# Optimization experiments

Measured on AMD Instinct MI355X. Metric: run time of the kernel, lower is better.

## Reference

```python
import jax, jax.numpy as jnp
import numpy as np

EPS_PHI = 1e-18  # weight assigned to neighbors outside the support radius


def setup_inputs() -> dict:
    key = jax.random.key(0)
    k1, k2, k3, k4 = jax.random.split(key, 4)
    N, P, K = 2, 100000, 60
    points = jax.random.normal(k1, (N, P, 3), dtype=jnp.float32)
    v = jax.random.normal(k2, (N, P, K, 3), dtype=jnp.float32)
    vn = jax.random.normal(k3, (N, P, K, 3), dtype=jnp.float32)
    # squared support radii: positive, bounded away from zero
    sr = jax.random.uniform(k4, (N, P, K), dtype=jnp.float32) + 0.1
    return {"points": points, "v": v, "vn": vn, "sr": sr}


def reference(points, v, vn, sr):
    # points: (N,P,3); v,vn: (N,P,K,3); sr: (N,P,K)
    p_v = points[:, :, None, :] - v                      # (N,P,K,3)
    dists = jnp.sum(p_v * p_v, axis=-1)                  # (N,P,K) squared distances
    inside = dists < sr                                  # (N,P,K)
    w = 1.0 - dists / sr
    phi_v = jnp.where(inside, (w * w) * (w * w), EPS_PHI)  # quartic kernel weight
    v_to_p_dot_n = jnp.sum(vn * p_v, axis=-1)            # (N,P,K)
    sdf = jnp.sum(phi_v * v_to_p_dot_n, axis=-1) / jnp.sum(phi_v, axis=-1)  # (N,P)
    return jnp.sum(sdf * sdf, axis=-1)                   # (N,)
```

## Files before the change

kernel.cpp:

```cpp
#include <hip/hip_runtime.h>

#define SLOTS 256

__global__ __launch_bounds__(256) void sdf_main(
    const float* __restrict__ points,
    const float* __restrict__ v,
    const float* __restrict__ vn,
    const float* __restrict__ sr,
    float* __restrict__ ws,
    int NP, int K, int P)
{
    const int wave = blockIdx.x * 4 + (threadIdx.x >> 6);
    const int lane = threadIdx.x & 63;
    if (wave >= NP) return;

    const float px = points[wave * 3 + 0];
    const float py = points[wave * 3 + 1];
    const float pz = points[wave * 3 + 2];

    float num = 0.0f, den = 0.0f;
    if (lane < K) {
        const int base = (wave * K + lane) * 3;
        const float vx = v[base + 0];
        const float vy = v[base + 1];
        const float vz = v[base + 2];
        const float nx = vn[base + 0];
        const float ny = vn[base + 1];
        const float nz = vn[base + 2];
        const float s  = sr[wave * K + lane];

        const float dx = px - vx;
        const float dy = py - vy;
        const float dz = pz - vz;
        const float d2 = dx * dx + dy * dy + dz * dz;
        const float w  = 1.0f - d2 / s;
        const float w2 = w * w;
        const float phi = (d2 < s) ? (w2 * w2) : 1e-18f;
        const float dot = nx * dx + ny * dy + nz * dz;
        num = phi * dot;
        den = phi;
    }

    #pragma unroll
    for (int off = 32; off >= 1; off >>= 1) {
        num += __shfl_xor(num, off, 64);
        den += __shfl_xor(den, off, 64);
    }

    if (lane == 0) {
        const float sdf = num / den;
        const int n = wave / P;
        const int slot = wave & (SLOTS - 1);
        atomicAdd(&ws[slot * 2 + n], sdf * sdf);
    }
}

__global__ __launch_bounds__(512) void sdf_reduce(
    const float* __restrict__ ws, float* __restrict__ out, int N)
{
    __shared__ float sm[2 * SLOTS];
    const int tid  = threadIdx.x;
    const int n    = tid >> 8;
    const int slot = tid & (SLOTS - 1);
    sm[tid] = (n < N) ? ws[slot * 2 + n] : 0.0f;
    __syncthreads();
    #pragma unroll
    for (int s = SLOTS / 2; s >= 1; s >>= 1) {
        if (slot < s) sm[tid] += sm[tid + s];
        __syncthreads();
    }
    if (slot == 0 && n < N) out[n] = sm[tid];
}

extern "C" void kernel_launch(void* const* d_in, const int* in_sizes, int n_in,
                              void* d_out, int out_size, void* d_ws, size_t ws_size,
                              hipStream_t stream) {
    const float* points = (const float*)d_in[0];
    const float* v      = (const float*)d_in[1];
    const float* vn     = (const float*)d_in[2];
    const float* sr     = (const float*)d_in[3];
    float* out = (float*)d_out;
    float* ws  = (float*)d_ws;

    const int NP = in_sizes[0] / 3;
    const int K  = in_sizes[3] / NP;
    const int N  = out_size;
    const int P  = NP / N;

    hipMemsetAsync(ws, 0, SLOTS * 2 * sizeof(float), stream);

    const int waves_needed = NP;
    const int blocks = (waves_needed + 3) / 4;
    sdf_main<<<blocks, 256, 0, stream>>>(points, v, vn, sr, ws, NP, K, P);
    sdf_reduce<<<1, 2 * SLOTS, 0, stream>>>(ws, out, N);
}
```

Baseline: 382.5 us.

## Stage neighbor data via coalesced float4 loads into LDS and pad atomic slots

Each wave now loads its point's v, vn and sr rows as contiguous float4 vectors into shared memory, then reads the strided xyz components from LDS. This replaces the stride-3 scalar global loads. The atomic accumulation buffer grows to 512 slots with a 64-byte stride to reduce atomic contention and false sharing, and the reduce kernel loops over the slots. K is hardcoded to 60, and a block-wide barrier is added.

```diff
diff --git a/kernel.cpp b/kernel.cpp
--- a/kernel.cpp
+++ b/kernel.cpp
@@ -1,6 +1,6 @@
 #include <hip/hip_runtime.h>
 
-#define SLOTS 256
+#define RED_THREADS 512
 
 __global__ __launch_bounds__(256) void sdf_main(
     const float* __restrict__ points,
@@ -8,33 +8,55 @@
     const float* __restrict__ vn,
     const float* __restrict__ sr,
     float* __restrict__ ws,
-    int NP, int K, int P)
+    int NP, int P, int slots, int slotStride)
 {
-    const int wave = blockIdx.x * 4 + (threadIdx.x >> 6);
-    const int lane = threadIdx.x & 63;
-    if (wave >= NP) return;
+    constexpr int K = 60;
+    __shared__ float4 sv[4][45];
+    __shared__ float4 sn[4][45];
+    __shared__ float4 ss[4][15];
 
-    const float px = points[wave * 3 + 0];
-    const float py = points[wave * 3 + 1];
-    const float pz = points[wave * 3 + 2];
+    const int w     = threadIdx.x >> 6;
+    const int lane  = threadIdx.x & 63;
+    const int point = blockIdx.x * 4 + w;
+    const bool active = point < NP;
 
-    float num = 0.0f, den = 0.0f;
-    if (lane < K) {
-        const int base = (wave * K + lane) * 3;
-        const float vx = v[base + 0];
-        const float vy = v[base + 1];
-        const float vz = v[base + 2];
-        const float nx = vn[base + 0];
-        const float ny = vn[base + 1];
-        const float nz = vn[base + 2];
-        const float s  = sr[wave * K + lane];
+    float px = 0.f, py = 0.f, pz = 0.f;
+    if (active) {
+        const float4* v4 = (const float4*)(v  + (size_t)point * (K * 3));
+        const float4* n4 = (const float4*)(vn + (size_t)point * (K * 3));
+        const float4* s4 = (const float4*)(sr + (size_t)point * K);
+        float4 rv, rn, rs;
+        if (lane < 45) rv = v4[lane];
+        if (lane < 45) rn = n4[lane];
+        if (lane < 15) rs = s4[lane];
+        px = points[point * 3 + 0];
+        py = points[point * 3 + 1];
+        pz = points[point * 3 + 2];
+        if (lane < 45) sv[w][lane] = rv;
+        if (lane < 45) sn[w][lane] = rn;
+        if (lane < 15) ss[w][lane] = rs;
+    }
+    __syncthreads();
+
+    float num = 0.f, den = 0.f;
+    if (active && lane < K) {
+        const float* vf = (const float*)sv[w];
+        const float* nf = (const float*)sn[w];
+        const float* sf = (const float*)ss[w];
+        const float vx = vf[3 * lane + 0];
+        const float vy = vf[3 * lane + 1];
+        const float vz = vf[3 * lane + 2];
+        const float nx = nf[3 * lane + 0];
+        const float ny = nf[3 * lane + 1];
+        const float nz = nf[3 * lane + 2];
+        const float s  = sf[lane];
 
         const float dx = px - vx;
         const float dy = py - vy;
         const float dz = pz - vz;
         const float d2 = dx * dx + dy * dy + dz * dz;
-        const float w  = 1.0f - d2 / s;
-        const float w2 = w * w;
+        const float wq = 1.0f - d2 / s;
+        const float w2 = wq * wq;
         const float phi = (d2 < s) ? (w2 * w2) : 1e-18f;
         const float dot = nx * dx + ny * dy + nz * dz;
         num = phi * dot;
@@ -47,29 +69,41 @@
         den += __shfl_xor(den, off, 64);
     }
 
-    if (lane == 0) {
+    if (active && lane == 0) {
         const float sdf = num / den;
-        const int n = wave / P;
-        const int slot = wave & (SLOTS - 1);
-        atomicAdd(&ws[slot * 2 + n], sdf * sdf);
+        const int n    = point / P;
+        const int slot = point & (slots - 1);
+        atomicAdd(&ws[slot * slotStride + n], sdf * sdf);
     }
 }
 
-__global__ __launch_bounds__(512) void sdf_reduce(
-    const float* __restrict__ ws, float* __restrict__ out, int N)
+__global__ __launch_bounds__(RED_THREADS) void sdf_reduce(
+    const float* __restrict__ ws, float* __restrict__ out,
+    int N, int slots, int slotStride)
 {
-    __shared__ float sm[2 * SLOTS];
-    const int tid  = threadIdx.x;
-    const int n    = tid >> 8;
-    const int slot = tid & (SLOTS - 1);
-    sm[tid] = (n < N) ? ws[slot * 2 + n] : 0.0f;
+    __shared__ float sm0[RED_THREADS];
+    __shared__ float sm1[RED_THREADS];
+    const int tid = threadIdx.x;
+    float a = 0.f, b = 0.f;
+    for (int s = tid; s < slots; s += RED_THREADS) {
+        a += ws[s * slotStride + 0];
+        if (N > 1) b += ws[s * slotStride + 1];
+    }
+    sm0[tid] = a;
+    sm1[tid] = b;
     __syncthreads();
     #pragma unroll
-    for (int s = SLOTS / 2; s >= 1; s >>= 1) {
-        if (slot < s) sm[tid] += sm[tid + s];
+    for (int s = RED_THREADS / 2; s >= 1; s >>= 1) {
+        if (tid < s) {
+            sm0[tid] += sm0[tid + s];
+            sm1[tid] += sm1[tid + s];
+        }
         __syncthreads();
     }
-    if (slot == 0 && n < N) out[n] = sm[tid];
+    if (tid == 0) {
+        out[0] = sm0[0];
+        if (N > 1) out[1] = sm1[0];
+    }
 }
 
 extern "C" void kernel_launch(void* const* d_in, const int* in_sizes, int n_in,
@@ -83,14 +117,18 @@
     float* ws  = (float*)d_ws;
 
     const int NP = in_sizes[0] / 3;
-    const int K  = in_sizes[3] / NP;
     const int N  = out_size;
     const int P  = NP / N;
 
-    hipMemsetAsync(ws, 0, SLOTS * 2 * sizeof(float), stream);
+    int slots = 512, slotStride = 16;
+    if (ws_size < (size_t)(slots * slotStride * sizeof(float))) {
+        slots = 256; slotStride = 2;
+    }
 
-    const int waves_needed = NP;
-    const int blocks = (waves_needed + 3) / 4;
-    sdf_main<<<blocks, 256, 0, stream>>>(points, v, vn, sr, ws, NP, K, P);
-    sdf_reduce<<<1, 2 * SLOTS, 0, stream>>>(ws, out, N);
+    hipMemsetAsync(ws, 0, (size_t)slots * slotStride * sizeof(float), stream);
+
+    const int blocks = (NP + 3) / 4;
+    sdf_main<<<blocks, 256, 0, stream>>>(points, v, vn, sr, ws, NP, P,
+                                         slots, slotStride);
+    sdf_reduce<<<1, RED_THREADS, 0, stream>>>(ws, out, N, slots, slotStride);
 }
```

After: 327.0 us. -14.5%, faster.
